# Kernel optimization log

Hardware: AMD Instinct MI355X
Metric: run time of the kernel (lower is better)

## Reference

```python
import jax, jax.numpy as jnp
import numpy as np

NUM_EXPERTS = 8
TOP_K = 2
INIT_STD = 0.02


def setup_inputs() -> dict:
    key = jax.random.key(0)
    k = jax.random.split(key, 6)
    B, S, D, F, E = 2, 2048, 768, 3072, NUM_EXPERTS
    hidden_states = jax.random.normal(k[0], (B, S, D), dtype=jnp.float32)
    gate_w = jax.random.normal(k[1], (D, E), dtype=jnp.float32) * (1.0 / np.sqrt(D))
    w_up = jax.random.normal(k[2], (E, D, F), dtype=jnp.float32) * INIT_STD
    b_up = jnp.zeros((E, F), dtype=jnp.float32)
    w_down = jax.random.normal(k[3], (E, F, D), dtype=jnp.float32) * INIT_STD
    b_down = jnp.zeros((E, D), dtype=jnp.float32)
    return {"hidden_states": hidden_states, "gate_w": gate_w, "w_up": w_up,
            "b_up": b_up, "w_down": w_down, "b_down": b_down}


def reference(hidden_states, gate_w, w_up, b_up, w_down, b_down):
    B, S, D = hidden_states.shape
    E = gate_w.shape[1]
    x = hidden_states.reshape(-1, D)                      # [T, D]
    T = x.shape[0]
    # Gate (eval mode: no noise, temperature 1.0)
    logits = x @ gate_w                                   # [T, E]
    probs = jax.nn.softmax(logits, axis=-1)
    top_w, top_i = jax.lax.top_k(probs, TOP_K)            # [T, K] (not renormalized)
    # Per-token combine weight for every expert (0 if not selected)
    combine = jnp.zeros((T, E), dtype=x.dtype).at[
        jnp.arange(T)[:, None], top_i].add(top_w)         # [T, E]
    # Dense all-expert FFN; masked combine reproduces sparse dispatch math
    h = jax.nn.gelu(jnp.einsum('td,edf->tef', x, w_up) + b_up, approximate=False)
    y = jnp.einsum('tef,efd->ted', h, w_down) + b_down[None, :, :]  # [T, E, D]
    out = jnp.einsum('ted,te->td', y, combine)            # [T, D]
    return out.reshape(B, S, D)
```

## Files before the change

### kernel.cpp

```cpp
#include <hip/hip_runtime.h>
#include <hip/hip_bf16.h>
#include <math.h>

#define T_TOKENS 4096
#define D_DIM 768
#define F_DIM 3072
#define E_NUM 8

#define BM 128
#define BN 128
#define BK 32
#define RBMAX 72
#define NBU (F_DIM / BN)
#define NBD (D_DIM / BN)
#define UP_BLOCKS (NBU * RBMAX)
#define DBM 64
#define DN_BLOCKS (NBD * RBMAX * 2)

#define TILE_LDS (64 * 66)
#define TRT_WUP 4608
#define TRT_TOT 9216

typedef __attribute__((ext_vector_type(8))) short short8;
typedef __attribute__((ext_vector_type(4))) short short4v;
typedef __attribute__((ext_vector_type(4))) float float4v;
typedef unsigned short ushort_t;

__device__ __forceinline__ ushort_t f2bf(float f) {
    union { float f; unsigned u; } v; v.f = f;
    unsigned r = v.u + 0x7fffu + ((v.u >> 16) & 1u);
    return (ushort_t)(r >> 16);
}

__device__ __forceinline__ float gelu_fast(float v) {
    float u = v + 0.044715f * v * v * v;
    return v / (1.f + __expf(-1.5957691216f * u));
}

#define GLOAD_LDS16(gp, lp) __builtin_amdgcn_global_load_lds( \
    (const __attribute__((address_space(1))) void*)(gp),      \
    (__attribute__((address_space(3))) void*)(lp), 16, 0, 0)

__device__ __forceinline__ void tile_coords(int g, int R, int C,
                                            int& e, int& r0, int& c0) {
    int tpr = C / 64, tpc = R / 64;
    e = g / (tpr * tpc);
    int rem = g % (tpr * tpc);
    r0 = (rem / tpr) * 64;
    c0 = (rem % tpr) * 64;
}

__device__ __forceinline__ void wave_transpose64(const float* __restrict__ ip,
                                                 ushort_t* __restrict__ op,
                                                 int R, int C, int r0, int c0,
                                                 ushort_t* __restrict__ tl) {
    int l = threadIdx.x & 63;
    int lr = l >> 4;
    int lc4 = (l & 15) * 4;

    float4v v[16];
#pragma unroll
    for (int i = 0; i < 16; ++i)
        v[i] = *(const float4v*)&ip[(size_t)(r0 + 4 * i + lr) * C + c0 + lc4];
#pragma unroll
    for (int i = 0; i < 16; ++i) {
        short4v s = { (short)f2bf(v[i][0]), (short)f2bf(v[i][1]),
                      (short)f2bf(v[i][2]), (short)f2bf(v[i][3]) };
        *(short4v*)&tl[(4 * i + lr) * 66 + lc4] = s;
    }
    asm volatile("s_waitcnt lgkmcnt(0)" ::: "memory");
#pragma unroll
    for (int i = 0; i < 16; ++i) {
        int rr = 4 * i + lr;
        short4v s = { (short)tl[(lc4 + 0) * 66 + rr],
                      (short)tl[(lc4 + 1) * 66 + rr],
                      (short)tl[(lc4 + 2) * 66 + rr],
                      (short)tl[(lc4 + 3) * 66 + rr] };
        *(short4v*)&op[(size_t)(c0 + rr) * R + r0 + lc4] = s;
    }
}

__global__ __launch_bounds__(256) void k_trans(const float* __restrict__ wup,
                                               const float* __restrict__ wdn,
                                               ushort_t* __restrict__ wupT,
                                               ushort_t* __restrict__ wdnT) {
    __shared__ ushort_t ttile[4][TILE_LDS];
    int wave = threadIdx.x >> 6;
    int g = blockIdx.x * 4 + wave;
    const float* in; ushort_t* outp; int R, C;
    if (g < TRT_WUP) { in = wup; outp = wupT; R = D_DIM; C = F_DIM; }
    else { g -= TRT_WUP; in = wdn; outp = wdnT; R = F_DIM; C = D_DIM; }
    int e, r0, c0;
    tile_coords(g, R, C, e, r0, c0);
    wave_transpose64(in + (size_t)e * R * C, outp + (size_t)e * R * C,
                     R, C, r0, c0, &ttile[wave][0]);
}

__global__ __launch_bounds__(1024) void k_gate(const float* __restrict__ x,
                                               const float* __restrict__ gw,
                                               int* __restrict__ counts,
                                               int* __restrict__ list,
                                               float* __restrict__ wsel) {
    __shared__ int hist[E_NUM];
    __shared__ int base[E_NUM];
    int wave = threadIdx.x >> 6, lane = threadIdx.x & 63;
    int t = blockIdx.x * 16 + wave;

    float acc[E_NUM];
#pragma unroll
    for (int e = 0; e < E_NUM; ++e) acc[e] = 0.f;
    const float* xr = x + (size_t)t * D_DIM;
    for (int d = lane; d < D_DIM; d += 64) {
        float xv = xr[d];
        const float* g = gw + d * E_NUM;
#pragma unroll
        for (int e = 0; e < E_NUM; ++e) acc[e] += xv * g[e];
    }
#pragma unroll
    for (int e = 0; e < E_NUM; ++e) {
#pragma unroll
        for (int s = 32; s >= 1; s >>= 1) acc[e] += __shfl_xor(acc[e], s);
    }

    if (threadIdx.x < E_NUM) hist[threadIdx.x] = 0;
    __syncthreads();

    int e1 = 0, e2 = 0, s1 = 0, s2 = 0;
    if (lane == 0) {
        float mx = acc[0];
#pragma unroll
        for (int e = 1; e < E_NUM; ++e) mx = fmaxf(mx, acc[e]);
        float p[E_NUM], sum = 0.f;
#pragma unroll
        for (int e = 0; e < E_NUM; ++e) { p[e] = expf(acc[e] - mx); sum += p[e]; }
        float inv = 1.f / sum;
#pragma unroll
        for (int e = 0; e < E_NUM; ++e) p[e] *= inv;
#pragma unroll
        for (int e = 1; e < E_NUM; ++e) if (p[e] > p[e1]) e1 = e;
        e2 = (e1 == 0) ? 1 : 0;
#pragma unroll
        for (int e = 0; e < E_NUM; ++e) if (e != e1 && p[e] > p[e2]) e2 = e;
        s1 = atomicAdd(&hist[e1], 1);
        s2 = atomicAdd(&hist[e2], 1);
        wsel[t * 2 + 0] = p[e1];
        wsel[t * 2 + 1] = p[e2];
    }
    __syncthreads();
    if (threadIdx.x < E_NUM)
        base[threadIdx.x] = atomicAdd(&counts[threadIdx.x], hist[threadIdx.x]);
    __syncthreads();
    if (lane == 0) {
        list[e1 * T_TOKENS + base[e1] + s1] = t * 2 + 0;
        list[e2 * T_TOKENS + base[e2] + s2] = t * 2 + 1;
    }
}

__global__ __launch_bounds__(256) void k_cvt(const float* __restrict__ x,
                                             ushort_t* __restrict__ xb) {
    int n4 = T_TOKENS * D_DIM / 4;
    for (int j = blockIdx.x * 256 + threadIdx.x; j < n4; j += 256 * 256) {
        float4v v = ((const float4v*)x)[j];
        unsigned long long o =
            (unsigned long long)f2bf(v[0]) |
            ((unsigned long long)f2bf(v[1]) << 16) |
            ((unsigned long long)f2bf(v[2]) << 32) |
            ((unsigned long long)f2bf(v[3]) << 48);
        ((unsigned long long*)xb)[j] = o;
    }
}

__global__ void k_finalize(const int* __restrict__ counts, int* __restrict__ pcount,
                           int* __restrict__ offs, int* __restrict__ nrb,
                           int* __restrict__ rbmap) {
    if (threadIdx.x == 0) {
        int acc = 0, rb = 0;
        for (int e = 0; e < E_NUM; ++e) {
            int pc = (counts[e] + BM - 1) / BM * BM;
            pcount[e] = pc;
            offs[e] = acc;
            for (int i = 0; i < pc / BM; ++i) rbmap[rb++] = e;
            acc += pc;
        }
        nrb[0] = rb;
    }
}

__global__ void k_compact(const int* __restrict__ counts, const int* __restrict__ pcount,
                          const int* __restrict__ offs, const int* __restrict__ list,
                          int* __restrict__ clist, int* __restrict__ rowOf) {
    int e = blockIdx.y;
    int s = blockIdx.x * 256 + threadIdx.x;
    if (s >= pcount[e]) return;
    int g = offs[e] + s;
    if (s < counts[e]) {
        int v = list[e * T_TOKENS + s];
        clist[g] = v >> 1;
        rowOf[v] = g;
    } else {
        clist[g] = 0;
    }
}

__global__ void k_up_gemm(const ushort_t* __restrict__ xb, const ushort_t* __restrict__ wupT,
                          const float* __restrict__ b_up, const int* __restrict__ nrb,
                          const int* __restrict__ rbmap, const int* __restrict__ clist,
                          ushort_t* __restrict__ h) {
    int wg = blockIdx.x;
    int lin = (wg & 7) * (UP_BLOCKS / 8) + (wg >> 3);
    int nb = lin / RBMAX;
    int rb = lin % RBMAX;
    if (rb >= nrb[0]) return;
    int e = rbmap[rb];
    __shared__ __align__(16) ushort_t As[2][BM][BK];
    __shared__ __align__(16) ushort_t Bs[2][BN][BK];
    int t = threadIdx.x, wave = t >> 6, lane = t & 63;
    int wm = wave >> 1, wn = wave & 1;

    int row0 = rb * BM;
    int tokA0 = clist[row0 + (t >> 2)];
    int tokA1 = clist[row0 + 64 + (t >> 2)];
    const ushort_t* wb = wupT + (size_t)e * F_DIM * D_DIM + (size_t)(nb * BN) * D_DIM;

    float4v acc[4][4];
#pragma unroll
    for (int i = 0; i < 4; ++i)
#pragma unroll
        for (int j = 0; j < 4; ++j)
#pragma unroll
            for (int q = 0; q < 4; ++q) acc[i][j][q] = 0.f;

    int csw = (((t & 3) ^ ((t >> 3) & 3))) * 8;
    int swoff = (((lane >> 4) ^ (((lane & 15) >> 1) & 3))) * 8;

    const ushort_t* gA0 = xb + (size_t)tokA0 * D_DIM + csw;
    const ushort_t* gA1 = xb + (size_t)tokA1 * D_DIM + csw;
    const ushort_t* gB0 = wb + (size_t)(t >> 2) * D_DIM + csw;
    const ushort_t* gB1 = wb + (size_t)(64 + (t >> 2)) * D_DIM + csw;

#define STAGE_UP(buf, kt) do { int k0 = (kt) * BK;                            \
        char* AsB = (char*)&As[buf][0][0]; char* BsB = (char*)&Bs[buf][0][0]; \
        GLOAD_LDS16(gA0 + k0, AsB + wave * 1024);                             \
        GLOAD_LDS16(gA1 + k0, AsB + 4096 + wave * 1024);                      \
        GLOAD_LDS16(gB0 + k0, BsB + wave * 1024);                             \
        GLOAD_LDS16(gB1 + k0, BsB + 4096 + wave * 1024); } while (0)

    STAGE_UP(0, 0);
    __syncthreads();
    const int nt = D_DIM / BK;
    for (int kt = 0; kt < nt; ++kt) {
        int buf = kt & 1;
        if (kt + 1 < nt) STAGE_UP(buf ^ 1, kt + 1);
        short8 af[4], bfr[4];
#pragma unroll
        for (int m = 0; m < 4; ++m)
            af[m] = *(const short8*)&As[buf][wm * 64 + m * 16 + (lane & 15)][swoff];
#pragma unroll
        for (int n = 0; n < 4; ++n)
            bfr[n] = *(const short8*)&Bs[buf][wn * 64 + n * 16 + (lane & 15)][swoff];
#pragma unroll
        for (int m = 0; m < 4; ++m)
#pragma unroll
            for (int n = 0; n < 4; ++n)
                acc[m][n] = __builtin_amdgcn_mfma_f32_16x16x32_bf16(af[m], bfr[n], acc[m][n], 0, 0, 0);
        __syncthreads();
    }

#pragma unroll
    for (int m = 0; m < 4; ++m) {
        int row_local = wm * 64 + m * 16 + (lane >> 4) * 4;
#pragma unroll
        for (int n = 0; n < 4; ++n) {
            int col = nb * BN + wn * 64 + n * 16 + (lane & 15);
            float bia = b_up[e * F_DIM + col];
#pragma unroll
            for (int j = 0; j < 4; ++j) {
                float v = acc[m][n][j] + bia;
                h[(size_t)(row0 + row_local + j) * F_DIM + col] = f2bf(gelu_fast(v));
            }
        }
    }
}

__global__ void k_down_gemm(const ushort_t* __restrict__ h, const ushort_t* __restrict__ wdT,
                            const float* __restrict__ b_down, const int* __restrict__ nrb,
                            const int* __restrict__ rbmap, float* __restrict__ yb) {
    int wg = blockIdx.x;
    int lin = (wg & 7) * (DN_BLOCKS / 8) + (wg >> 3);
    int nb = lin / (RBMAX * 2);
    int rbD = lin % (RBMAX * 2);
    if ((rbD >> 1) >= nrb[0]) return;
    int e = rbmap[rbD >> 1];
    __shared__ __align__(16) ushort_t As[2][DBM][BK];
    __shared__ __align__(16) ushort_t Bs[2][BN][BK];
    int t = threadIdx.x, wave = t >> 6, lane = t & 63;
    int wm = wave >> 1, wn = wave & 1;

    int row0 = rbD * DBM;
    const ushort_t* ha = h + (size_t)row0 * F_DIM;
    const ushort_t* wb = wdT + (size_t)e * D_DIM * F_DIM + (size_t)(nb * BN) * F_DIM;

    float4v acc[2][4];
#pragma unroll
    for (int i = 0; i < 2; ++i)
#pragma unroll
        for (int j = 0; j < 4; ++j)
#pragma unroll
            for (int q = 0; q < 4; ++q) acc[i][j][q] = 0.f;

    int csw = (((t & 3) ^ ((t >> 3) & 3))) * 8;
    int swoff = (((lane >> 4) ^ (((lane & 15) >> 1) & 3))) * 8;

    const ushort_t* gA0 = ha + (size_t)(t >> 2) * F_DIM + csw;
    const ushort_t* gB0 = wb + (size_t)(t >> 2) * F_DIM + csw;
    const ushort_t* gB1 = wb + (size_t)(64 + (t >> 2)) * F_DIM + csw;

#define STAGE_DN(buf, kt) do { int k0 = (kt) * BK;                            \
        char* AsB = (char*)&As[buf][0][0]; char* BsB = (char*)&Bs[buf][0][0]; \
        GLOAD_LDS16(gA0 + k0, AsB + wave * 1024);                             \
        GLOAD_LDS16(gB0 + k0, BsB + wave * 1024);                             \
        GLOAD_LDS16(gB1 + k0, BsB + 4096 + wave * 1024); } while (0)

    STAGE_DN(0, 0);
    __syncthreads();
    const int nt = F_DIM / BK;
    for (int kt = 0; kt < nt; ++kt) {
        int buf = kt & 1;
        if (kt + 1 < nt) STAGE_DN(buf ^ 1, kt + 1);
        short8 af[2], bfr[4];
#pragma unroll
        for (int m = 0; m < 2; ++m)
            af[m] = *(const short8*)&As[buf][wm * 32 + m * 16 + (lane & 15)][swoff];
#pragma unroll
        for (int n = 0; n < 4; ++n)
            bfr[n] = *(const short8*)&Bs[buf][wn * 64 + n * 16 + (lane & 15)][swoff];
#pragma unroll
        for (int m = 0; m < 2; ++m)
#pragma unroll
            for (int n = 0; n < 4; ++n)
                acc[m][n] = __builtin_amdgcn_mfma_f32_16x16x32_bf16(af[m], bfr[n], acc[m][n], 0, 0, 0);
        __syncthreads();
    }

#pragma unroll
    for (int m = 0; m < 2; ++m) {
        int row_local = wm * 32 + m * 16 + (lane >> 4) * 4;
#pragma unroll
        for (int n = 0; n < 4; ++n) {
            int col = nb * BN + wn * 64 + n * 16 + (lane & 15);
            float bia = b_down[e * D_DIM + col];
#pragma unroll
            for (int j = 0; j < 4; ++j) {
                yb[(size_t)(row0 + row_local + j) * D_DIM + col] = acc[m][n][j] + bia;
            }
        }
    }
}

__global__ void k_combine(const float* __restrict__ yb, const int* __restrict__ rowOf,
                          const float* __restrict__ wsel, float* __restrict__ out) {
    int wave = threadIdx.x >> 6, lane = threadIdx.x & 63;
    int t = blockIdx.x * 4 + wave;
    int g0 = rowOf[t * 2], g1 = rowOf[t * 2 + 1];
    float w0 = wsel[t * 2], w1 = wsel[t * 2 + 1];
    const float4v* y0 = (const float4v*)(yb + (size_t)g0 * D_DIM);
    const float4v* y1 = (const float4v*)(yb + (size_t)g1 * D_DIM);
    float4v* o = (float4v*)(out + (size_t)t * D_DIM);
#pragma unroll
    for (int i = 0; i < 3; ++i) {
        int idx = lane + i * 64;
        float4v a = y0[idx], b = y1[idx];
        float4v r;
#pragma unroll
        for (int q = 0; q < 4; ++q) r[q] = w0 * a[q] + w1 * b[q];
        o[idx] = r;
    }
}

extern "C" void kernel_launch(void* const* d_in, const int* in_sizes, int n_in,
                              void* d_out, int out_size, void* d_ws, size_t ws_size,
                              hipStream_t stream) {
    const float* x   = (const float*)d_in[0];
    const float* gw  = (const float*)d_in[1];
    const float* wup = (const float*)d_in[2];
    const float* bup = (const float*)d_in[3];
    const float* wdn = (const float*)d_in[4];
    const float* bdn = (const float*)d_in[5];
    float* out = (float*)d_out;

    char* ws = (char*)d_ws;
    int*   counts = (int*)(ws);
    int*   pcount = (int*)(ws + 32);
    int*   offs   = (int*)(ws + 64);
    int*   nrb    = (int*)(ws + 96);
    int*   rbmap  = (int*)(ws + 128);
    int*   list   = (int*)(ws + 1024);
    size_t p = 1024 + (size_t)E_NUM * T_TOKENS * 4;
    int*   clist  = (int*)(ws + p); p += (size_t)(RBMAX * BM) * 4;
    int*   rowOf  = (int*)(ws + p); p += (size_t)T_TOKENS * 2 * 4;
    float* wsel   = (float*)(ws + p); p += (size_t)T_TOKENS * 2 * 4;
    p = (p + 255) & ~(size_t)255;
    size_t p_xb = p;
    ushort_t* xb   = (ushort_t*)(ws + p); p += (size_t)T_TOKENS * D_DIM * 2;
    ushort_t* wupT = (ushort_t*)(ws + p); p += (size_t)E_NUM * D_DIM * F_DIM * 2;
    ushort_t* wdnT = (ushort_t*)(ws + p); p += (size_t)E_NUM * D_DIM * F_DIM * 2;
    ushort_t* hbuf = (ushort_t*)(ws + p); p += (size_t)(RBMAX * BM) * F_DIM * 2;
    float* ybuf = (float*)(ws + p_xb);

    hipMemsetAsync(counts, 0, E_NUM * sizeof(int), stream);
    k_gate<<<T_TOKENS / 16, 1024, 0, stream>>>(x, gw, counts, list, wsel);
    k_trans<<<TRT_TOT / 4, 256, 0, stream>>>(wup, wdn, wupT, wdnT);
    k_cvt<<<256, 256, 0, stream>>>(x, xb);
    k_finalize<<<1, 64, 0, stream>>>(counts, pcount, offs, nrb, rbmap);
    k_compact<<<dim3(T_TOKENS / 256, E_NUM), 256, 0, stream>>>(
        counts, pcount, offs, list, clist, rowOf);
    k_up_gemm<<<UP_BLOCKS, 256, 0, stream>>>(
        xb, wupT, bup, nrb, rbmap, clist, hbuf);
    k_down_gemm<<<DN_BLOCKS, 256, 0, stream>>>(
        hbuf, wdnT, bdn, nrb, rbmap, ybuf);
    k_combine<<<T_TOKENS / 4, 256, 0, stream>>>(ybuf, rowOf, wsel, out);
}
```

Measured before the change: 234.6 us.

## Split-K down GEMM with bf16 partials, fuse cvt into gate, drop finalize

The fp32-to-bf16 conversion of x now happens inside the gate kernel, replacing the separate k_cvt pass. The k_finalize kernel is removed: the GEMM and compact kernels work out each row block's expert and offsets directly from counts. The down GEMM is split into two K halves, doubling the block count to fill the GPU better. Each half writes bf16 partials, which k_combine adds together, so there are fewer launches and less traffic on the output buffer. The cost is extra rounding, since down-projection partials are now stored in bf16 instead of fp32, plus more reads in combine.

```diff
diff --git a/kernel.cpp b/kernel.cpp
--- a/kernel.cpp
+++ b/kernel.cpp
@@ -15,7 +15,9 @@
 #define NBD (D_DIM / BN)
 #define UP_BLOCKS (NBU * RBMAX)
 #define DBM 64
-#define DN_BLOCKS (NBD * RBMAX * 2)
+#define KHALF (F_DIM / 2)
+#define DN_BLOCKS (NBD * RBMAX * 2 * 2)
+#define GROWS (RBMAX * BM)
 
 #define TILE_LDS (64 * 66)
 #define TRT_WUP 4608
@@ -25,6 +27,7 @@
 typedef __attribute__((ext_vector_type(4))) short short4v;
 typedef __attribute__((ext_vector_type(4))) float float4v;
 typedef unsigned short ushort_t;
+typedef unsigned long long ull_t;
 
 __device__ __forceinline__ ushort_t f2bf(float f) {
     union { float f; unsigned u; } v; v.f = f;
@@ -32,6 +35,11 @@
     return (ushort_t)(r >> 16);
 }
 
+__device__ __forceinline__ float bf2f(ushort_t u) {
+    union { unsigned u; float f; } v; v.u = ((unsigned)u) << 16;
+    return v.f;
+}
+
 __device__ __forceinline__ float gelu_fast(float v) {
     float u = v + 0.044715f * v * v * v;
     return v / (1.f + __expf(-1.5957691216f * u));
@@ -40,6 +48,19 @@
 #define GLOAD_LDS16(gp, lp) __builtin_amdgcn_global_load_lds( \
     (const __attribute__((address_space(1))) void*)(gp),      \
     (__attribute__((address_space(3))) void*)(lp), 16, 0, 0)
+
+__device__ __forceinline__ int rb_expert(const int* __restrict__ counts,
+                                         int rb, int& total) {
+    int e = 0, acc = 0;
+#pragma unroll
+    for (int ee = 0; ee < E_NUM; ++ee) {
+        int nbe = (counts[ee] + BM - 1) / BM;
+        if (rb >= acc && rb < acc + nbe) e = ee;
+        acc += nbe;
+    }
+    total = acc;
+    return e;
+}
 
 __device__ __forceinline__ void tile_coords(int g, int R, int C,
                                             int& e, int& r0, int& c0) {
@@ -100,7 +121,8 @@
                                                const float* __restrict__ gw,
                                                int* __restrict__ counts,
                                                int* __restrict__ list,
-                                               float* __restrict__ wsel) {
+                                               float* __restrict__ wsel,
+                                               ushort_t* __restrict__ xb) {
     __shared__ int hist[E_NUM];
     __shared__ int base[E_NUM];
     int wave = threadIdx.x >> 6, lane = threadIdx.x & 63;
@@ -109,12 +131,21 @@
     float acc[E_NUM];
 #pragma unroll
     for (int e = 0; e < E_NUM; ++e) acc[e] = 0.f;
-    const float* xr = x + (size_t)t * D_DIM;
-    for (int d = lane; d < D_DIM; d += 64) {
-        float xv = xr[d];
-        const float* g = gw + d * E_NUM;
-#pragma unroll
-        for (int e = 0; e < E_NUM; ++e) acc[e] += xv * g[e];
+    const float4v* xr4 = (const float4v*)(x + (size_t)t * D_DIM);
+    ull_t* xbr = (ull_t*)(xb + (size_t)t * D_DIM);
+#pragma unroll
+    for (int i = 0; i < 3; ++i) {
+        int j = lane + i * 64;
+        float4v v = xr4[j];
+        xbr[j] = (ull_t)f2bf(v[0]) | ((ull_t)f2bf(v[1]) << 16) |
+                 ((ull_t)f2bf(v[2]) << 32) | ((ull_t)f2bf(v[3]) << 48);
+        int d0 = 4 * j;
+#pragma unroll
+        for (int q = 0; q < 4; ++q) {
+            const float* g = gw + (size_t)(d0 + q) * E_NUM;
+#pragma unroll
+            for (int e = 0; e < E_NUM; ++e) acc[e] += v[q] * g[e];
+        }
     }
 #pragma unroll
     for (int e = 0; e < E_NUM; ++e) {
@@ -156,44 +187,22 @@
     }
 }
 
-__global__ __launch_bounds__(256) void k_cvt(const float* __restrict__ x,
-                                             ushort_t* __restrict__ xb) {
-    int n4 = T_TOKENS * D_DIM / 4;
-    for (int j = blockIdx.x * 256 + threadIdx.x; j < n4; j += 256 * 256) {
-        float4v v = ((const float4v*)x)[j];
-        unsigned long long o =
-            (unsigned long long)f2bf(v[0]) |
-            ((unsigned long long)f2bf(v[1]) << 16) |
-            ((unsigned long long)f2bf(v[2]) << 32) |
-            ((unsigned long long)f2bf(v[3]) << 48);
-        ((unsigned long long*)xb)[j] = o;
-    }
-}
-
-__global__ void k_finalize(const int* __restrict__ counts, int* __restrict__ pcount,
-                           int* __restrict__ offs, int* __restrict__ nrb,
-                           int* __restrict__ rbmap) {
-    if (threadIdx.x == 0) {
-        int acc = 0, rb = 0;
-        for (int e = 0; e < E_NUM; ++e) {
-            int pc = (counts[e] + BM - 1) / BM * BM;
-            pcount[e] = pc;
-            offs[e] = acc;
-            for (int i = 0; i < pc / BM; ++i) rbmap[rb++] = e;
-            acc += pc;
-        }
-        nrb[0] = rb;
-    }
-}
-
-__global__ void k_compact(const int* __restrict__ counts, const int* __restrict__ pcount,
-                          const int* __restrict__ offs, const int* __restrict__ list,
+__global__ void k_compact(const int* __restrict__ counts, const int* __restrict__ list,
                           int* __restrict__ clist, int* __restrict__ rowOf) {
     int e = blockIdx.y;
     int s = blockIdx.x * 256 + threadIdx.x;
-    if (s >= pcount[e]) return;
-    int g = offs[e] + s;
-    if (s < counts[e]) {
+    int off = 0, cnt = 0;
+#pragma unroll
+    for (int ee = 0; ee < E_NUM; ++ee) {
+        int c = counts[ee];
+        int pc = (c + BM - 1) / BM * BM;
+        if (ee < e) off += pc;
+        if (ee == e) cnt = c;
+    }
+    int pcnt = (cnt + BM - 1) / BM * BM;
+    if (s >= pcnt) return;
+    int g = off + s;
+    if (s < cnt) {
         int v = list[e * T_TOKENS + s];
         clist[g] = v >> 1;
         rowOf[v] = g;
@@ -203,15 +212,15 @@
 }
 
 __global__ void k_up_gemm(const ushort_t* __restrict__ xb, const ushort_t* __restrict__ wupT,
-                          const float* __restrict__ b_up, const int* __restrict__ nrb,
-                          const int* __restrict__ rbmap, const int* __restrict__ clist,
-                          ushort_t* __restrict__ h) {
+                          const float* __restrict__ b_up, const int* __restrict__ counts,
+                          const int* __restrict__ clist, ushort_t* __restrict__ h) {
     int wg = blockIdx.x;
     int lin = (wg & 7) * (UP_BLOCKS / 8) + (wg >> 3);
     int nb = lin / RBMAX;
     int rb = lin % RBMAX;
-    if (rb >= nrb[0]) return;
-    int e = rbmap[rb];
+    int total;
+    int e = rb_expert(counts, rb, total);
+    if (rb >= total) return;
     __shared__ __align__(16) ushort_t As[2][BM][BK];
     __shared__ __align__(16) ushort_t Bs[2][BN][BK];
     int t = threadIdx.x, wave = t >> 6, lane = t & 63;
@@ -283,22 +292,26 @@
 }
 
 __global__ void k_down_gemm(const ushort_t* __restrict__ h, const ushort_t* __restrict__ wdT,
-                            const float* __restrict__ b_down, const int* __restrict__ nrb,
-                            const int* __restrict__ rbmap, float* __restrict__ yb) {
+                            const float* __restrict__ b_down, const int* __restrict__ counts,
+                            ushort_t* __restrict__ yb) {
     int wg = blockIdx.x;
     int lin = (wg & 7) * (DN_BLOCKS / 8) + (wg >> 3);
-    int nb = lin / (RBMAX * 2);
+    int nbkc = lin / (RBMAX * 2);
     int rbD = lin % (RBMAX * 2);
-    if ((rbD >> 1) >= nrb[0]) return;
-    int e = rbmap[rbD >> 1];
+    int nb = nbkc >> 1, kc = nbkc & 1;
+    int rb = rbD >> 1;
+    int total;
+    int e = rb_expert(counts, rb, total);
+    if (rb >= total) return;
     __shared__ __align__(16) ushort_t As[2][DBM][BK];
     __shared__ __align__(16) ushort_t Bs[2][BN][BK];
     int t = threadIdx.x, wave = t >> 6, lane = t & 63;
     int wm = wave >> 1, wn = wave & 1;
 
     int row0 = rbD * DBM;
-    const ushort_t* ha = h + (size_t)row0 * F_DIM;
-    const ushort_t* wb = wdT + (size_t)e * D_DIM * F_DIM + (size_t)(nb * BN) * F_DIM;
+    int kbase = kc * KHALF;
+    const ushort_t* ha = h + (size_t)row0 * F_DIM + kbase;
+    const ushort_t* wb = wdT + (size_t)e * D_DIM * F_DIM + (size_t)(nb * BN) * F_DIM + kbase;
 
     float4v acc[2][4];
 #pragma unroll
@@ -323,7 +336,7 @@
 
     STAGE_DN(0, 0);
     __syncthreads();
-    const int nt = F_DIM / BK;
+    const int nt = KHALF / BK;
     for (int kt = 0; kt < nt; ++kt) {
         int buf = kt & 1;
         if (kt + 1 < nt) STAGE_DN(buf ^ 1, kt + 1);
@@ -342,38 +355,47 @@
         __syncthreads();
     }
 
+    ushort_t* ybk = yb + (size_t)kc * GROWS * D_DIM;
 #pragma unroll
     for (int m = 0; m < 2; ++m) {
         int row_local = wm * 32 + m * 16 + (lane >> 4) * 4;
 #pragma unroll
         for (int n = 0; n < 4; ++n) {
             int col = nb * BN + wn * 64 + n * 16 + (lane & 15);
-            float bia = b_down[e * D_DIM + col];
+            float bia = (kc == 0) ? b_down[e * D_DIM + col] : 0.f;
 #pragma unroll
             for (int j = 0; j < 4; ++j) {
-                yb[(size_t)(row0 + row_local + j) * D_DIM + col] = acc[m][n][j] + bia;
+                ybk[(size_t)(row0 + row_local + j) * D_DIM + col] =
+                    f2bf(acc[m][n][j] + bia);
             }
         }
     }
 }
 
-__global__ void k_combine(const float* __restrict__ yb, const int* __restrict__ rowOf,
+__global__ void k_combine(const ushort_t* __restrict__ yb, const int* __restrict__ rowOf,
                           const float* __restrict__ wsel, float* __restrict__ out) {
     int wave = threadIdx.x >> 6, lane = threadIdx.x & 63;
     int t = blockIdx.x * 4 + wave;
     int g0 = rowOf[t * 2], g1 = rowOf[t * 2 + 1];
     float w0 = wsel[t * 2], w1 = wsel[t * 2 + 1];
-    const float4v* y0 = (const float4v*)(yb + (size_t)g0 * D_DIM);
-    const float4v* y1 = (const float4v*)(yb + (size_t)g1 * D_DIM);
+    const ushort_t* a0 = yb + (size_t)g0 * D_DIM;
+    const ushort_t* a1 = yb + ((size_t)GROWS + g0) * D_DIM;
+    const ushort_t* b0 = yb + (size_t)g1 * D_DIM;
+    const ushort_t* b1 = yb + ((size_t)GROWS + g1) * D_DIM;
     float4v* o = (float4v*)(out + (size_t)t * D_DIM);
 #pragma unroll
     for (int i = 0; i < 3; ++i) {
-        int idx = lane + i * 64;
-        float4v a = y0[idx], b = y1[idx];
+        int idx = (lane + i * 64) * 4;
+        short4v va0 = *(const short4v*)&a0[idx];
+        short4v va1 = *(const short4v*)&a1[idx];
+        short4v vb0 = *(const short4v*)&b0[idx];
+        short4v vb1 = *(const short4v*)&b1[idx];
         float4v r;
 #pragma unroll
-        for (int q = 0; q < 4; ++q) r[q] = w0 * a[q] + w1 * b[q];
-        o[idx] = r;
+        for (int q = 0; q < 4; ++q)
+            r[q] = w0 * (bf2f((ushort_t)va0[q]) + bf2f((ushort_t)va1[q]))
+                 + w1 * (bf2f((ushort_t)vb0[q]) + bf2f((ushort_t)vb1[q]));
+        o[(lane + i * 64)] = r;
     }
 }
 
@@ -390,13 +412,9 @@
 
     char* ws = (char*)d_ws;
     int*   counts = (int*)(ws);
-    int*   pcount = (int*)(ws + 32);
-    int*   offs   = (int*)(ws + 64);
-    int*   nrb    = (int*)(ws + 96);
-    int*   rbmap  = (int*)(ws + 128);
     int*   list   = (int*)(ws + 1024);
     size_t p = 1024 + (size_t)E_NUM * T_TOKENS * 4;
-    int*   clist  = (int*)(ws + p); p += (size_t)(RBMAX * BM) * 4;
+    int*   clist  = (int*)(ws + p); p += (size_t)GROWS * 4;
     int*   rowOf  = (int*)(ws + p); p += (size_t)T_TOKENS * 2 * 4;
     float* wsel   = (float*)(ws + p); p += (size_t)T_TOKENS * 2 * 4;
     p = (p + 255) & ~(size_t)255;
@@ -404,19 +422,14 @@
     ushort_t* xb   = (ushort_t*)(ws + p); p += (size_t)T_TOKENS * D_DIM * 2;
     ushort_t* wupT = (ushort_t*)(ws + p); p += (size_t)E_NUM * D_DIM * F_DIM * 2;
     ushort_t* wdnT = (ushort_t*)(ws + p); p += (size_t)E_NUM * D_DIM * F_DIM * 2;
-    ushort_t* hbuf = (ushort_t*)(ws + p); p += (size_t)(RBMAX * BM) * F_DIM * 2;
-    float* ybuf = (float*)(ws + p_xb);
+    ushort_t* hbuf = (ushort_t*)(ws + p); p += (size_t)GROWS * F_DIM * 2;
+    ushort_t* ybuf = (ushort_t*)(ws + p_xb);
 
     hipMemsetAsync(counts, 0, E_NUM * sizeof(int), stream);
-    k_gate<<<T_TOKENS / 16, 1024, 0, stream>>>(x, gw, counts, list, wsel);
+    k_gate<<<T_TOKENS / 16, 1024, 0, stream>>>(x, gw, counts, list, wsel, xb);
     k_trans<<<TRT_TOT / 4, 256, 0, stream>>>(wup, wdn, wupT, wdnT);
-    k_cvt<<<256, 256, 0, stream>>>(x, xb);
-    k_finalize<<<1, 64, 0, stream>>>(counts, pcount, offs, nrb, rbmap);
-    k_compact<<<dim3(T_TOKENS / 256, E_NUM), 256, 0, stream>>>(
-        counts, pcount, offs, list, clist, rowOf);
-    k_up_gemm<<<UP_BLOCKS, 256, 0, stream>>>(
-        xb, wupT, bup, nrb, rbmap, clist, hbuf);
-    k_down_gemm<<<DN_BLOCKS, 256, 0, stream>>>(
-        hbuf, wdnT, bdn, nrb, rbmap, ybuf);
+    k_compact<<<dim3(17, E_NUM), 256, 0, stream>>>(counts, list, clist, rowOf);
+    k_up_gemm<<<UP_BLOCKS, 256, 0, stream>>>(xb, wupT, bup, counts, clist, hbuf);
+    k_down_gemm<<<DN_BLOCKS, 256, 0, stream>>>(hbuf, wdnT, bdn, counts, ybuf);
     k_combine<<<T_TOKENS / 4, 256, 0, stream>>>(ybuf, rowOf, wsel, out);
 }
```

Measured after the change: 227.9 us. -2.8%, faster.
